# Performance work log

Measured on AMD Instinct MI355X. Metric: run time of the kernel, lower is better.

Reference implementation:

```python
import jax, jax.numpy as jnp
import numpy as np

HEAD_SIZE = 64


def setup_inputs() -> dict:
    key = jax.random.key(0)
    k1, k2, k3, k4 = jax.random.split(key, 4)
    x = jax.random.normal(k1, (4, 4096, 1024), dtype=jnp.float32)
    Wk = jax.random.normal(k2, (1024, HEAD_SIZE), dtype=jnp.float32) * 0.02
    Wq = jax.random.normal(k3, (1024, HEAD_SIZE), dtype=jnp.float32) * 0.02
    Wv = jax.random.normal(k4, (1024, HEAD_SIZE), dtype=jnp.float32) * 0.02
    return {"x": x, "Wk": Wk, "Wq": Wq, "Wv": Wv}


def reference(x, Wk, Wq, Wv):
    # x: [B, S, D]; projections (Linear without bias): x @ W -> [B, S, H]
    k = jnp.einsum('bsd,dh->bsh', x, Wk)
    q = jnp.einsum('bsd,dh->bsh', x, Wq)
    v = jnp.einsum('bsd,dh->bsh', x, Wv)
    scale = 1.0 / np.sqrt(HEAD_SIZE).astype(np.float32)
    z = jnp.einsum('bqh,bkh->bqk', q, k) * scale  # [B, S, S]
    S = x.shape[1]
    causal = jnp.tril(jnp.ones((S, S), dtype=bool))
    z = jnp.where(causal, z, -jnp.inf)
    z = jax.nn.softmax(z, axis=2)
    return jnp.einsum('bqk,bkh->bqh', z, v)
```

## Files before the change

kernel.cpp:

```cpp
#include <hip/hip_runtime.h>
#include <hip/hip_bf16.h>
#include <stdint.h>
#include <math.h>

typedef __attribute__((ext_vector_type(8))) short short8;
typedef __attribute__((ext_vector_type(4))) short short4v;
typedef __attribute__((ext_vector_type(4))) float float4v;

#define MFMA16(a,b,c) __builtin_amdgcn_mfma_f32_16x16x32_bf16((a),(b),(c),0,0,0)
#define MFMA16K16(a,b,c) __builtin_amdgcn_mfma_f32_16x16x16bf16_1k((a),(b),(c),0,0,0)

__device__ __forceinline__ short bf16r(float f) {
  union { float f; uint32_t u; } v; v.f = f;
  uint32_t r = v.u + 0x7fffu + ((v.u >> 16) & 1u);
  return (short)(r >> 16);
}
__device__ __forceinline__ float bf2f(short s) {
  union { float f; uint32_t u; } v; v.u = ((uint32_t)(uint16_t)s) << 16;
  return v.f;
}
__device__ __forceinline__ uint32_t cvtpk(float a, float b) {
  uint32_t r;
  asm("v_cvt_pk_bf16_f32 %0, %1, %2" : "=v"(r) : "v"(a), "v"(b));
  return r;
}

__device__ __forceinline__ void gld_lds16(void* lds, const void* g) {
  __builtin_amdgcn_global_load_lds(
      (const __attribute__((address_space(1))) uint32_t*)g,
      (__attribute__((address_space(3))) uint32_t*)lds, 16, 0, 0);
}

__global__ __launch_bounds__(256) void prep_wt(
    const float* __restrict__ Wk, const float* __restrict__ Wq,
    const float* __restrict__ Wv, short* __restrict__ WT) {
  __shared__ float tile[64][65];
  const int w = blockIdx.y;
  const int k0 = blockIdx.x * 64;
  const float* W = (w == 0) ? Wk : (w == 1) ? Wq : Wv;
  const int tid = threadIdx.x;
#pragma unroll
  for (int i = 0; i < 16; ++i) {
    int e = i * 256 + tid;
    int kk = e >> 6, hh = e & 63;
    tile[kk][hh] = W[(size_t)(k0 + kk) * 64 + hh];
  }
  __syncthreads();
#pragma unroll
  for (int i = 0; i < 16; ++i) {
    int e = i * 256 + tid;
    int hh = e >> 6, kk = e & 63;
    WT[(size_t)w * 65536 + hh * 1024 + k0 + kk] = bf16r(tile[kk][hh]);
  }
}

__global__ __launch_bounds__(512, 4) void proj_kernel(
    const float* __restrict__ x, const short* __restrict__ WT,
    short* __restrict__ Kg, short* __restrict__ Qg, short* __restrict__ Vt) {
  __shared__ __align__(16) short xs[2][32][72];
  __shared__ __align__(16) short wts[2][192 * 64];
  const int tid = threadIdx.x;
  const int lane = tid & 63;
  const int w = tid >> 6;
  const int c = lane & 15;
  const int sl = lane >> 4;
  const int mh = w & 1;
  const int nh = w >> 1;
  const int m0 = blockIdx.x * 32;

  float4v acc[3];
#pragma unroll
  for (int ni = 0; ni < 3; ++ni) acc[ni] = (float4v){0.f, 0.f, 0.f, 0.f};

  const int srow = tid >> 4;
  const int scol = (tid & 15) * 4;
  const float* xrow = x + (size_t)(m0 + srow) * 1024 + scol;

#define PSTAGE_WT(buf, kk)                                                    \
  _Pragma("unroll") for (int rr = 0; rr < 3; ++rr) {                          \
    const int chunk = rr * 512 + tid;                                         \
    const int n = chunk >> 3;                                                 \
    const int cc = chunk & 7;                                                 \
    gld_lds16(wts[buf] + chunk * 8,                                           \
              WT + (size_t)n * 1024 + (kk) + ((cc ^ (n & 7)) * 8));           \
  }
#define PWRITE_X(buf)                                                         \
  {                                                                           \
    short4v hx;                                                               \
    hx.x = bf16r(xr.x); hx.y = bf16r(xr.y);                                   \
    hx.z = bf16r(xr.z); hx.w = bf16r(xr.w);                                   \
    *(short4v*)(&xs[buf][srow][scol]) = hx;                                   \
  }

  float4v xr = *(const float4v*)(xrow);
  float4v xn = *(const float4v*)(xrow + 64);

  PSTAGE_WT(0, 0)
  PWRITE_X(0)
  __syncthreads();

  int cur = 0;
  for (int it = 0; it < 16; ++it) {
    const int k0 = it * 64;
    if (it + 1 < 16) {
      PSTAGE_WT(cur ^ 1, k0 + 64)
      xr = xn;
      PWRITE_X(cur ^ 1)
      if (it + 2 < 16) xn = *(const float4v*)(xrow + k0 + 128);
    }
    short8 a0 = *(const short8*)(&xs[cur][mh * 16 + c][sl * 8]);
    short8 a1 = *(const short8*)(&xs[cur][mh * 16 + c][32 + sl * 8]);
#pragma unroll
    for (int ni = 0; ni < 3; ++ni) {
      const int rw = (nh * 3 + ni) * 16 + c;
      short8 b0 = *(const short8*)(wts[cur] + rw * 64 + ((sl ^ (rw & 7)) * 8));
      short8 b1 = *(const short8*)(wts[cur] + rw * 64 + (((sl + 4) ^ (rw & 7)) * 8));
      acc[ni] = MFMA16(a0, b0, acc[ni]);
      acc[ni] = MFMA16(a1, b1, acc[ni]);
    }
    __syncthreads();
    cur ^= 1;
  }
#undef PSTAGE_WT
#undef PWRITE_X

  const int b = m0 >> 12;
  const int s_base = m0 & 4095;
  const float QSCALE = 0.18033688011112042f;
#pragma unroll
  for (int ni = 0; ni < 3; ++ni) {
    const int nt = nh * 3 + ni;
    const int wsel = nt >> 2;
    const int h = (nt & 3) * 16 + c;
    const int q_local = mh * 16 + sl * 4;
    if (wsel == 2) {
      short4v pv;
      pv.x = bf16r(acc[ni].x); pv.y = bf16r(acc[ni].y);
      pv.z = bf16r(acc[ni].z); pv.w = bf16r(acc[ni].w);
      *(short4v*)(Vt + (size_t)(b * 64 + h) * 4096 + s_base + q_local) = pv;
    } else if (wsel == 1) {
#pragma unroll
      for (int i = 0; i < 4; ++i)
        Qg[(size_t)(m0 + q_local + i) * 64 + h] = bf16r(acc[ni][i] * QSCALE);
    } else {
#pragma unroll
      for (int i = 0; i < 4; ++i)
        Kg[(size_t)(m0 + q_local + i) * 64 + h] = bf16r(acc[ni][i]);
    }
  }
}

#define SLOT_BYTES 16896
__global__ __launch_bounds__(512, 4) void attn_kernel(
    const short* __restrict__ Qg, const short* __restrict__ Kg,
    const short* __restrict__ Vt, float* __restrict__ out,
    char* __restrict__ part, int split) {
  __shared__ __align__(16) short Ks[4][64 * 64];
  __shared__ __align__(16) short Vs[4][64 * 64];
  const int tid = threadIdx.x;
  const int lane = tid & 63;
  const int w = tid >> 6;
  const int c = lane & 15;
  const int sl = lane >> 4;

  int g, ch, b, uu = 0;
  if (split) {
    const int lin = (blockIdx.x & 7) * 136 + (blockIdx.x >> 3);
    b = lin / 272;
    uu = lin - b * 272;
    g = (int)(2.0f * sqrtf((float)uu));
    while (((g + 2) >> 1) * ((g + 3) >> 1) <= uu) ++g;
    while (((g + 1) >> 1) * ((g + 2) >> 1) > uu) --g;
    ch = uu - ((g + 1) >> 1) * ((g + 2) >> 1);
  } else { g = blockIdx.x; b = blockIdx.y; ch = 0; }
  const int T = 2 * (g + 1);
  const int c0 = ch * 4;
  const int c1 = (!split || c0 + 4 > T) ? T : c0 + 4;
  const int nch = split ? ((g >> 1) + 1) : 1;
  const int nt_loc = c1 - c0;
  const int qw = g * 128 + w * 16;

  const short* Kb = Kg + (size_t)b * 4096 * 64;
  const short* Vb = Vt + (size_t)b * 64 * 4096;

  short8 aq0, aq1;
  {
    const short* qp = Qg + (size_t)(b * 4096 + qw + c) * 64 + sl * 8;
    aq0 = *(const short8*)(qp);
    aq1 = *(const short8*)(qp + 32);
  }

  float4v o[4];
#pragma unroll
  for (int ht = 0; ht < 4; ++ht) o[ht] = (float4v){0.f, 0.f, 0.f, 0.f};
  float4v osum = {0.f, 0.f, 0.f, 0.f};

  union { uint32_t u[2]; short4v s4; } one_init;
  one_init.u[0] = 0x3F803F80u;
  one_init.u[1] = 0x3F803F80u;
  const short4v vones = one_init.s4;

  {
    const int rw = tid >> 3;
    const int scol = ((tid & 7) ^ (rw & 7)) * 8;
#pragma unroll
    for (int tt = 0; tt < 4; ++tt) {
      if (tt < nt_loc) {
        const int kv0s = (c0 + tt) * 64;
        gld_lds16(Ks[tt] + tid * 8, Kb + (size_t)(kv0s + rw) * 64 + scol);
        gld_lds16(Vs[tt] + tid * 8, Vb + (size_t)rw * 4096 + kv0s + scol);
      }
    }
  }
  __syncthreads();

  for (int tt = 0; tt < nt_loc; ++tt) {
    const int kv0 = (c0 + tt) * 64;
    const short* KsC = Ks[tt];
    const short* VsC = Vs[tt];

    float4v s[4];
    __builtin_amdgcn_s_setprio(1);
#pragma unroll
    for (int nt = 0; nt < 4; ++nt) {
      const int rw = nt * 16 + c;
      short8 kb0 = *(const short8*)(KsC + rw * 64 + ((sl ^ (rw & 7)) * 8));
      short8 kb1 = *(const short8*)(KsC + rw * 64 + (((sl + 4) ^ (rw & 7)) * 8));
      float4v z = {0.f, 0.f, 0.f, 0.f};
      z = MFMA16(kb0, aq0, z);
      z = MFMA16(kb1, aq1, z);
      s[nt] = z;
    }
    __builtin_amdgcn_s_setprio(0);

    if (kv0 + 63 > qw) {
      const int qg = qw + c;
#pragma unroll
      for (int nt = 0; nt < 4; ++nt)
#pragma unroll
        for (int i = 0; i < 4; ++i) {
          const int kvg = kv0 + nt * 16 + sl * 4 + i;
          s[nt][i] = (kvg <= qg) ? s[nt][i] : -1e30f;
        }
    }

    short4v pa[4];
#pragma unroll
    for (int nt = 0; nt < 4; ++nt) {
      const float p0 = exp2f(s[nt][0]);
      const float p1 = exp2f(s[nt][1]);
      const float p2 = exp2f(s[nt][2]);
      const float p3 = exp2f(s[nt][3]);
      union { uint32_t u[2]; short4v s4; } cv;
      cv.u[0] = cvtpk(p0, p1);
      cv.u[1] = cvtpk(p2, p3);
      pa[nt] = cv.s4;
    }

    __builtin_amdgcn_s_setprio(1);
#pragma unroll
    for (int ht = 0; ht < 4; ++ht) {
      const int row = ht * 16 + c;
#pragma unroll
      for (int nt = 0; nt < 4; ++nt) {
        const int slot8 = (nt * 2 + (sl >> 1)) ^ (row & 7);
        short4v vb = *(const short4v*)(VsC + row * 64 + slot8 * 8 + (sl & 1) * 4);
        o[ht] = MFMA16K16(pa[nt], vb, o[ht]);
      }
    }
#pragma unroll
    for (int nt = 0; nt < 4; ++nt)
      osum = MFMA16K16(pa[nt], vones, osum);
    __builtin_amdgcn_s_setprio(0);
  }

  if (nch == 1) {
    float inv[4];
#pragma unroll
    for (int i = 0; i < 4; ++i) inv[i] = 1.0f / osum[i];
#pragma unroll
    for (int ht = 0; ht < 4; ++ht)
#pragma unroll
      for (int i = 0; i < 4; ++i) {
        const int q = qw + sl * 4 + i;
        out[(size_t)(b * 4096 + q) * 64 + ht * 16 + c] = o[ht][i] * inv[i];
      }
  } else {
    short* sp = (short*)(part + (size_t)(b * 272 + uu) * SLOT_BYTES);
    float* lp = (float*)(sp + 8192);
#pragma unroll
    for (int ht = 0; ht < 4; ++ht)
#pragma unroll
      for (int i = 0; i < 4; ++i) {
        const int row = w * 16 + sl * 4 + i;
        sp[row * 64 + ht * 16 + c] = bf16r(o[ht][i]);
      }
    if (c == 0) {
#pragma unroll
      for (int i = 0; i < 4; ++i)
        lp[w * 16 + sl * 4 + i] = osum[i];
    }
  }
}

__global__ __launch_bounds__(256) void combine_kernel(
    const char* __restrict__ part, float* __restrict__ out) {
  const int g = blockIdx.x;
  const int b = blockIdx.y;
  const int N = (g >> 1) + 1;
  if (N == 1) return;
  const int F = ((g + 1) >> 1) * ((g + 2) >> 1);
  const char* base = part + (size_t)(b * 272 + F) * SLOT_BYTES;
  const int r = blockIdx.z * 32 + (threadIdx.x >> 3);
  const int cb = (threadIdx.x & 7) * 8;

  float L = 0.f;
  float acc[8];
#pragma unroll
  for (int k = 0; k < 8; ++k) acc[k] = 0.f;
  for (int i = 0; i < N; ++i) {
    const short* sp = (const short*)(base + (size_t)i * SLOT_BYTES);
    L += ((const float*)(sp + 8192))[r];
    short8 v = *(const short8*)(sp + r * 64 + cb);
#pragma unroll
    for (int j = 0; j < 8; ++j) acc[j] += bf2f(v[j]);
  }
  const float inv = 1.0f / L;
  float* op = out + (size_t)(b * 4096 + g * 128 + r) * 64 + cb;
  float4v r0 = {acc[0] * inv, acc[1] * inv, acc[2] * inv, acc[3] * inv};
  float4v r1 = {acc[4] * inv, acc[5] * inv, acc[6] * inv, acc[7] * inv};
  *(float4v*)(op) = r0;
  *(float4v*)(op + 4) = r1;
}

extern "C" void kernel_launch(void* const* d_in, const int* in_sizes, int n_in,
                              void* d_out, int out_size, void* d_ws, size_t ws_size,
                              hipStream_t stream) {
  const float* x  = (const float*)d_in[0];
  const float* Wk = (const float*)d_in[1];
  const float* Wq = (const float*)d_in[2];
  const float* Wv = (const float*)d_in[3];

  char* ws = (char*)d_ws;
  short* WT = (short*)ws;
  short* Kg = (short*)(ws + 393216);
  short* Qg = (short*)(ws + 393216 + 2097152);
  short* Vt = (short*)(ws + 393216 + 2 * 2097152);
  const size_t part_off = 393216 + 3 * 2097152;
  char* part = ws + part_off;

  const int split = (ws_size >= part_off + (size_t)1088 * SLOT_BYTES) ? 1 : 0;

  prep_wt<<<dim3(16, 3), dim3(256), 0, stream>>>(Wk, Wq, Wv, WT);
  proj_kernel<<<dim3(512), dim3(512), 0, stream>>>(x, WT, Kg, Qg, Vt);
  attn_kernel<<<split ? dim3(1088) : dim3(32, 4), dim3(512), 0, stream>>>(
      Qg, Kg, Vt, (float*)d_out, part, split);
  if (split)
    combine_kernel<<<dim3(32, 4, 4), dim3(256), 0, stream>>>(part, (float*)d_out);
}
```

Baseline: 56.77 us.

## Fuse split-KV combine into attention kernel via last-block atomic counter

Removes the separate combine kernel launch. Each split block writes its bf16 partial output and row sums, then increments a per-(batch, query-group) atomic counter with release/acquire fences, and the last block to arrive reduces all partials and writes the final output. This saves a kernel launch and its tail, but adds a memset for the counters and leaves the reduction serialized on the last block of each group.

```diff
diff --git a/kernel.cpp b/kernel.cpp
--- a/kernel.cpp
+++ b/kernel.cpp
@@ -154,9 +154,10 @@
 __global__ __launch_bounds__(512, 4) void attn_kernel(
     const short* __restrict__ Qg, const short* __restrict__ Kg,
     const short* __restrict__ Vt, float* __restrict__ out,
-    char* __restrict__ part, int split) {
+    char* __restrict__ part, int* __restrict__ cnt, int split) {
   __shared__ __align__(16) short Ks[4][64 * 64];
   __shared__ __align__(16) short Vs[4][64 * 64];
+  __shared__ int lastFlag;
   const int tid = threadIdx.x;
   const int lane = tid & 63;
   const int w = tid >> 6;
@@ -285,52 +286,64 @@
         const int q = qw + sl * 4 + i;
         out[(size_t)(b * 4096 + q) * 64 + ht * 16 + c] = o[ht][i] * inv[i];
       }
-  } else {
-    short* sp = (short*)(part + (size_t)(b * 272 + uu) * SLOT_BYTES);
-    float* lp = (float*)(sp + 8192);
-#pragma unroll
-    for (int ht = 0; ht < 4; ++ht)
-#pragma unroll
-      for (int i = 0; i < 4; ++i) {
-        const int row = w * 16 + sl * 4 + i;
-        sp[row * 64 + ht * 16 + c] = bf16r(o[ht][i]);
-      }
-    if (c == 0) {
-#pragma unroll
-      for (int i = 0; i < 4; ++i)
-        lp[w * 16 + sl * 4 + i] = osum[i];
-    }
-  }
-}
-
-__global__ __launch_bounds__(256) void combine_kernel(
-    const char* __restrict__ part, float* __restrict__ out) {
-  const int g = blockIdx.x;
-  const int b = blockIdx.y;
-  const int N = (g >> 1) + 1;
-  if (N == 1) return;
+    return;
+  }
+
+  short* sp = (short*)(part + (size_t)(b * 272 + uu) * SLOT_BYTES);
+  float* lp = (float*)(sp + 8192);
+#pragma unroll
+  for (int ht = 0; ht < 4; ++ht)
+#pragma unroll
+    for (int i = 0; i < 4; ++i) {
+      const int row = w * 16 + sl * 4 + i;
+      sp[row * 64 + ht * 16 + c] = bf16r(o[ht][i]);
+    }
+  if (c == 0) {
+#pragma unroll
+    for (int i = 0; i < 4; ++i)
+      lp[w * 16 + sl * 4 + i] = osum[i];
+  }
+
+  __syncthreads();
+  if (tid == 0) {
+    __builtin_amdgcn_fence(__ATOMIC_RELEASE, "agent");
+    int old = __hip_atomic_fetch_add(&cnt[b * 32 + g], 1,
+                                     __ATOMIC_RELAXED, __HIP_MEMORY_SCOPE_AGENT);
+    lastFlag = (old == nch - 1);
+  }
+  __syncthreads();
+  if (!lastFlag) return;
+  __builtin_amdgcn_fence(__ATOMIC_ACQUIRE, "agent");
+
   const int F = ((g + 1) >> 1) * ((g + 2) >> 1);
   const char* base = part + (size_t)(b * 272 + F) * SLOT_BYTES;
-  const int r = blockIdx.z * 32 + (threadIdx.x >> 3);
-  const int cb = (threadIdx.x & 7) * 8;
+  const int r = tid >> 2;
+  const int cb = (tid & 3) * 16;
 
   float L = 0.f;
-  float acc[8];
-#pragma unroll
-  for (int k = 0; k < 8; ++k) acc[k] = 0.f;
-  for (int i = 0; i < N; ++i) {
-    const short* sp = (const short*)(base + (size_t)i * SLOT_BYTES);
-    L += ((const float*)(sp + 8192))[r];
-    short8 v = *(const short8*)(sp + r * 64 + cb);
-#pragma unroll
-    for (int j = 0; j < 8; ++j) acc[j] += bf2f(v[j]);
+  float acc[16];
+#pragma unroll
+  for (int k = 0; k < 16; ++k) acc[k] = 0.f;
+  for (int i = 0; i < nch; ++i) {
+    const short* spp = (const short*)(base + (size_t)i * SLOT_BYTES);
+    L += ((const float*)(spp + 8192))[r];
+    const short* sr = spp + r * 64 + cb;
+    short8 v0 = *(const short8*)(sr);
+    short8 v1 = *(const short8*)(sr + 8);
+#pragma unroll
+    for (int j = 0; j < 8; ++j) {
+      acc[j] += bf2f(v0[j]);
+      acc[8 + j] += bf2f(v1[j]);
+    }
   }
   const float inv = 1.0f / L;
   float* op = out + (size_t)(b * 4096 + g * 128 + r) * 64 + cb;
-  float4v r0 = {acc[0] * inv, acc[1] * inv, acc[2] * inv, acc[3] * inv};
-  float4v r1 = {acc[4] * inv, acc[5] * inv, acc[6] * inv, acc[7] * inv};
-  *(float4v*)(op) = r0;
-  *(float4v*)(op + 4) = r1;
+#pragma unroll
+  for (int k = 0; k < 4; ++k) {
+    float4v res = {acc[k * 4] * inv, acc[k * 4 + 1] * inv,
+                   acc[k * 4 + 2] * inv, acc[k * 4 + 3] * inv};
+    *(float4v*)(op + k * 4) = res;
+  }
 }
 
 extern "C" void kernel_launch(void* const* d_in, const int* in_sizes, int n_in,
@@ -348,13 +361,14 @@
   short* Vt = (short*)(ws + 393216 + 2 * 2097152);
   const size_t part_off = 393216 + 3 * 2097152;
   char* part = ws + part_off;
-
-  const int split = (ws_size >= part_off + (size_t)1088 * SLOT_BYTES) ? 1 : 0;
+  const size_t cnt_off = part_off + (size_t)1088 * SLOT_BYTES;
+  int* cnt = (int*)(ws + cnt_off);
+
+  const int split = (ws_size >= cnt_off + 512) ? 1 : 0;
 
   prep_wt<<<dim3(16, 3), dim3(256), 0, stream>>>(Wk, Wq, Wv, WT);
+  if (split) hipMemsetAsync(cnt, 0, 512, stream);
   proj_kernel<<<dim3(512), dim3(512), 0, stream>>>(x, WT, Kg, Qg, Vt);
   attn_kernel<<<split ? dim3(1088) : dim3(32, 4), dim3(512), 0, stream>>>(
-      Qg, Kg, Vt, (float*)d_out, part, split);
-  if (split)
-    combine_kernel<<<dim3(32, 4, 4), dim3(256), 0, stream>>>(part, (float*)d_out);
-}
+      Qg, Kg, Vt, (float*)d_out, part, cnt, split);
+}
```

New measurement: 95.55 us. 1.68x slower.

## Process 32 query rows per wave to reuse K/V LDS reads across two fragments

Applied to the files above, without the earlier changes.

Each wave now handles two 16-row query fragments (256 queries per block) instead of one, so every K and V fragment read from LDS feeds two sets of MFMAs. The split-KV work decomposition is rebuilt from a 272-chunk scheme to a 136-chunk triangular scheme per batch, with larger partial slots and a combine kernel that covers 256-row groups. This halves LDS read traffic per MFMA and the number of blocks, at the cost of doubled accumulator registers (risking occupancy under the 4-block launch bound), fewer blocks for load balance, and more wasted masked work on diagonal tiles.

```diff
diff --git a/kernel.cpp b/kernel.cpp
--- a/kernel.cpp
+++ b/kernel.cpp
@@ -150,7 +150,7 @@
   }
 }
 
-#define SLOT_BYTES 16896
+#define SLOT_BYTES 33792
 __global__ __launch_bounds__(512, 4) void attn_kernel(
     const short* __restrict__ Qg, const short* __restrict__ Kg,
     const short* __restrict__ Vt, float* __restrict__ out,
@@ -165,35 +165,40 @@
 
   int g, ch, b, uu = 0;
   if (split) {
-    const int lin = (blockIdx.x & 7) * 136 + (blockIdx.x >> 3);
-    b = lin / 272;
-    uu = lin - b * 272;
-    g = (int)(2.0f * sqrtf((float)uu));
-    while (((g + 2) >> 1) * ((g + 3) >> 1) <= uu) ++g;
-    while (((g + 1) >> 1) * ((g + 2) >> 1) > uu) --g;
-    ch = uu - ((g + 1) >> 1) * ((g + 2) >> 1);
+    const int lin = (blockIdx.x & 7) * 68 + (blockIdx.x >> 3);
+    b = lin / 136;
+    uu = lin - b * 136;
+    g = (int)(0.5f * (sqrtf(8.0f * (float)uu + 1.0f) - 1.0f));
+    while ((g + 1) * (g + 2) / 2 <= uu) ++g;
+    while (g * (g + 1) / 2 > uu) --g;
+    ch = uu - g * (g + 1) / 2;
   } else { g = blockIdx.x; b = blockIdx.y; ch = 0; }
-  const int T = 2 * (g + 1);
+  const int T = 4 * (g + 1);
   const int c0 = ch * 4;
-  const int c1 = (!split || c0 + 4 > T) ? T : c0 + 4;
-  const int nch = split ? ((g >> 1) + 1) : 1;
+  const int c1 = split ? (c0 + 4) : T;
+  const int nch = split ? (g + 1) : 1;
   const int nt_loc = c1 - c0;
-  const int qw = g * 128 + w * 16;
+  const int qw = g * 256 + w * 32;
 
   const short* Kb = Kg + (size_t)b * 4096 * 64;
   const short* Vb = Vt + (size_t)b * 64 * 4096;
 
-  short8 aq0, aq1;
-  {
-    const short* qp = Qg + (size_t)(b * 4096 + qw + c) * 64 + sl * 8;
-    aq0 = *(const short8*)(qp);
-    aq1 = *(const short8*)(qp + 32);
-  }
-
-  float4v o[4];
-#pragma unroll
-  for (int ht = 0; ht < 4; ++ht) o[ht] = (float4v){0.f, 0.f, 0.f, 0.f};
-  float4v osum = {0.f, 0.f, 0.f, 0.f};
+  short8 aq[2][2];
+#pragma unroll
+  for (int qf = 0; qf < 2; ++qf) {
+    const short* qp = Qg + (size_t)(b * 4096 + qw + qf * 16 + c) * 64 + sl * 8;
+    aq[qf][0] = *(const short8*)(qp);
+    aq[qf][1] = *(const short8*)(qp + 32);
+  }
+
+  float4v o[2][4];
+#pragma unroll
+  for (int qf = 0; qf < 2; ++qf)
+#pragma unroll
+    for (int ht = 0; ht < 4; ++ht) o[qf][ht] = (float4v){0.f, 0.f, 0.f, 0.f};
+  float4v osum[2];
+  osum[0] = (float4v){0.f, 0.f, 0.f, 0.f};
+  osum[1] = (float4v){0.f, 0.f, 0.f, 0.f};
 
   union { uint32_t u[2]; short4v s4; } one_init;
   one_init.u[0] = 0x3F803F80u;
@@ -219,43 +224,51 @@
     const short* KsC = Ks[tt];
     const short* VsC = Vs[tt];
 
-    float4v s[4];
+    float4v s[2][4];
     __builtin_amdgcn_s_setprio(1);
 #pragma unroll
     for (int nt = 0; nt < 4; ++nt) {
       const int rw = nt * 16 + c;
       short8 kb0 = *(const short8*)(KsC + rw * 64 + ((sl ^ (rw & 7)) * 8));
       short8 kb1 = *(const short8*)(KsC + rw * 64 + (((sl + 4) ^ (rw & 7)) * 8));
-      float4v z = {0.f, 0.f, 0.f, 0.f};
-      z = MFMA16(kb0, aq0, z);
-      z = MFMA16(kb1, aq1, z);
-      s[nt] = z;
+#pragma unroll
+      for (int qf = 0; qf < 2; ++qf) {
+        float4v z = {0.f, 0.f, 0.f, 0.f};
+        z = MFMA16(kb0, aq[qf][0], z);
+        z = MFMA16(kb1, aq[qf][1], z);
+        s[qf][nt] = z;
+      }
     }
     __builtin_amdgcn_s_setprio(0);
 
     if (kv0 + 63 > qw) {
-      const int qg = qw + c;
-#pragma unroll
-      for (int nt = 0; nt < 4; ++nt)
-#pragma unroll
-        for (int i = 0; i < 4; ++i) {
-          const int kvg = kv0 + nt * 16 + sl * 4 + i;
-          s[nt][i] = (kvg <= qg) ? s[nt][i] : -1e30f;
-        }
-    }
-
-    short4v pa[4];
-#pragma unroll
-    for (int nt = 0; nt < 4; ++nt) {
-      const float p0 = exp2f(s[nt][0]);
-      const float p1 = exp2f(s[nt][1]);
-      const float p2 = exp2f(s[nt][2]);
-      const float p3 = exp2f(s[nt][3]);
-      union { uint32_t u[2]; short4v s4; } cv;
-      cv.u[0] = cvtpk(p0, p1);
-      cv.u[1] = cvtpk(p2, p3);
-      pa[nt] = cv.s4;
-    }
+#pragma unroll
+      for (int qf = 0; qf < 2; ++qf) {
+        const int qg = qw + qf * 16 + c;
+#pragma unroll
+        for (int nt = 0; nt < 4; ++nt)
+#pragma unroll
+          for (int i = 0; i < 4; ++i) {
+            const int kvg = kv0 + nt * 16 + sl * 4 + i;
+            s[qf][nt][i] = (kvg <= qg) ? s[qf][nt][i] : -1e30f;
+          }
+      }
+    }
+
+    short4v pa[2][4];
+#pragma unroll
+    for (int qf = 0; qf < 2; ++qf)
+#pragma unroll
+      for (int nt = 0; nt < 4; ++nt) {
+        const float p0 = exp2f(s[qf][nt][0]);
+        const float p1 = exp2f(s[qf][nt][1]);
+        const float p2 = exp2f(s[qf][nt][2]);
+        const float p3 = exp2f(s[qf][nt][3]);
+        union { uint32_t u[2]; short4v s4; } cv;
+        cv.u[0] = cvtpk(p0, p1);
+        cv.u[1] = cvtpk(p2, p3);
+        pa[qf][nt] = cv.s4;
+      }
 
     __builtin_amdgcn_s_setprio(1);
 #pragma unroll
@@ -265,40 +278,50 @@
       for (int nt = 0; nt < 4; ++nt) {
         const int slot8 = (nt * 2 + (sl >> 1)) ^ (row & 7);
         short4v vb = *(const short4v*)(VsC + row * 64 + slot8 * 8 + (sl & 1) * 4);
-        o[ht] = MFMA16K16(pa[nt], vb, o[ht]);
-      }
-    }
-#pragma unroll
-    for (int nt = 0; nt < 4; ++nt)
-      osum = MFMA16K16(pa[nt], vones, osum);
+        o[0][ht] = MFMA16K16(pa[0][nt], vb, o[0][ht]);
+        o[1][ht] = MFMA16K16(pa[1][nt], vb, o[1][ht]);
+      }
+    }
+#pragma unroll
+    for (int nt = 0; nt < 4; ++nt) {
+      osum[0] = MFMA16K16(pa[0][nt], vones, osum[0]);
+      osum[1] = MFMA16K16(pa[1][nt], vones, osum[1]);
+    }
     __builtin_amdgcn_s_setprio(0);
   }
 
   if (nch == 1) {
-    float inv[4];
-#pragma unroll
-    for (int i = 0; i < 4; ++i) inv[i] = 1.0f / osum[i];
-#pragma unroll
-    for (int ht = 0; ht < 4; ++ht)
-#pragma unroll
-      for (int i = 0; i < 4; ++i) {
-        const int q = qw + sl * 4 + i;
-        out[(size_t)(b * 4096 + q) * 64 + ht * 16 + c] = o[ht][i] * inv[i];
-      }
+#pragma unroll
+    for (int qf = 0; qf < 2; ++qf) {
+      float inv[4];
+#pragma unroll
+      for (int i = 0; i < 4; ++i) inv[i] = 1.0f / osum[qf][i];
+#pragma unroll
+      for (int ht = 0; ht < 4; ++ht)
+#pragma unroll
+        for (int i = 0; i < 4; ++i) {
+          const int q = qw + qf * 16 + sl * 4 + i;
+          out[(size_t)(b * 4096 + q) * 64 + ht * 16 + c] = o[qf][ht][i] * inv[i];
+        }
+    }
   } else {
-    short* sp = (short*)(part + (size_t)(b * 272 + uu) * SLOT_BYTES);
-    float* lp = (float*)(sp + 8192);
-#pragma unroll
-    for (int ht = 0; ht < 4; ++ht)
-#pragma unroll
-      for (int i = 0; i < 4; ++i) {
-        const int row = w * 16 + sl * 4 + i;
-        sp[row * 64 + ht * 16 + c] = bf16r(o[ht][i]);
-      }
+    short* sp = (short*)(part + (size_t)(b * 136 + uu) * SLOT_BYTES);
+    float* lp = (float*)(sp + 16384);
+#pragma unroll
+    for (int qf = 0; qf < 2; ++qf)
+#pragma unroll
+      for (int ht = 0; ht < 4; ++ht)
+#pragma unroll
+        for (int i = 0; i < 4; ++i) {
+          const int row = w * 32 + qf * 16 + sl * 4 + i;
+          sp[row * 64 + ht * 16 + c] = bf16r(o[qf][ht][i]);
+        }
     if (c == 0) {
 #pragma unroll
-      for (int i = 0; i < 4; ++i)
-        lp[w * 16 + sl * 4 + i] = osum[i];
+      for (int qf = 0; qf < 2; ++qf)
+#pragma unroll
+        for (int i = 0; i < 4; ++i)
+          lp[w * 32 + qf * 16 + sl * 4 + i] = osum[qf][i];
     }
   }
 }
@@ -307,10 +330,10 @@
     const char* __restrict__ part, float* __restrict__ out) {
   const int g = blockIdx.x;
   const int b = blockIdx.y;
-  const int N = (g >> 1) + 1;
+  const int N = g + 1;
   if (N == 1) return;
-  const int F = ((g + 1) >> 1) * ((g + 2) >> 1);
-  const char* base = part + (size_t)(b * 272 + F) * SLOT_BYTES;
+  const int F = g * (g + 1) / 2;
+  const char* base = part + (size_t)(b * 136 + F) * SLOT_BYTES;
   const int r = blockIdx.z * 32 + (threadIdx.x >> 3);
   const int cb = (threadIdx.x & 7) * 8;
 
@@ -320,13 +343,13 @@
   for (int k = 0; k < 8; ++k) acc[k] = 0.f;
   for (int i = 0; i < N; ++i) {
     const short* sp = (const short*)(base + (size_t)i * SLOT_BYTES);
-    L += ((const float*)(sp + 8192))[r];
+    L += ((const float*)(sp + 16384))[r];
     short8 v = *(const short8*)(sp + r * 64 + cb);
 #pragma unroll
     for (int j = 0; j < 8; ++j) acc[j] += bf2f(v[j]);
   }
   const float inv = 1.0f / L;
-  float* op = out + (size_t)(b * 4096 + g * 128 + r) * 64 + cb;
+  float* op = out + (size_t)(b * 4096 + g * 256 + r) * 64 + cb;
   float4v r0 = {acc[0] * inv, acc[1] * inv, acc[2] * inv, acc[3] * inv};
   float4v r1 = {acc[4] * inv, acc[5] * inv, acc[6] * inv, acc[7] * inv};
   *(float4v*)(op) = r0;
@@ -349,12 +372,12 @@
   const size_t part_off = 393216 + 3 * 2097152;
   char* part = ws + part_off;
 
-  const int split = (ws_size >= part_off + (size_t)1088 * SLOT_BYTES) ? 1 : 0;
+  const int split = (ws_size >= part_off + (size_t)544 * SLOT_BYTES) ? 1 : 0;
 
   prep_wt<<<dim3(16, 3), dim3(256), 0, stream>>>(Wk, Wq, Wv, WT);
   proj_kernel<<<dim3(512), dim3(512), 0, stream>>>(x, WT, Kg, Qg, Vt);
-  attn_kernel<<<split ? dim3(1088) : dim3(32, 4), dim3(512), 0, stream>>>(
+  attn_kernel<<<split ? dim3(544) : dim3(16, 4), dim3(512), 0, stream>>>(
       Qg, Kg, Vt, (float*)d_out, part, split);
   if (split)
-    combine_kernel<<<dim3(32, 4, 4), dim3(256), 0, stream>>>(part, (float*)d_out);
-}
+    combine_kernel<<<dim3(16, 4, 8), dim3(256), 0, stream>>>(part, (float*)d_out);
+}
```

After: 58.91 us. 3.8% more time.
